# Performance work log

Measured on AMD Instinct MI355X. Metric: run time of the kernel, lower is better.

The kernel has to match this reference:

```python
import jax, jax.numpy as jnp
import numpy as np

B, S, H, FFN, E = 2, 2048, 1024, 4096, 8

def setup_inputs() -> dict:
    key = jax.random.key(0)
    k0, k1, k2, k3 = jax.random.split(key, 4)
    return {
        "hidden_states": jax.random.normal(k0, (B, S, H), dtype=jnp.float32),
        "Wr": jax.random.normal(k1, (H, E), dtype=jnp.float32) * 0.02,
        "br": jnp.zeros((E,), dtype=jnp.float32),
        "W1": jax.random.normal(k2, (E, H, FFN), dtype=jnp.float32) * 0.02,
        "W2": jax.random.normal(k3, (E, FFN, H), dtype=jnp.float32) * 0.02,
    }

def reference(hidden_states, Wr, br, W1, W2):
    b, s, h = hidden_states.shape
    x = hidden_states.reshape(-1, h)                      # [T, H]
    # sinkhorn routing branch in forward: sigmoid activation then top-1
    route = jax.nn.sigmoid(x @ Wr + br)                   # [T, E]
    max_prob = jnp.max(route, axis=1, keepdims=True)      # [T, 1]
    max_ind = jnp.argmax(route, axis=1)                   # [T] int
    out = jnp.zeros_like(x)
    n_experts = Wr.shape[1]
    for e in range(n_experts):  # small fixed expert set
        mask = (max_ind == e)[:, None].astype(x.dtype)    # [T, 1] dispatch mask
        # expert MLP: fc2(gelu(fc1(x))), no bias (add_bias_linear=False)
        y = jax.nn.gelu(x @ W1[e], approximate=False) @ W2[e]  # [T, H]
        out = out + mask * y                              # scatter-combine
    out = out * max_prob                                  # scale by router prob
    return out.reshape(b, s, h)
```

## Files before the change

### kernel.cpp

```cpp
#include <hip/hip_runtime.h>
#include <hip/hip_bf16.h>
#include <math.h>

#define TOK 4096
#define HD 1024
#define FD 4096
#define NE 8

typedef __attribute__((ext_vector_type(4))) float f32x4;
typedef __attribute__((ext_vector_type(8))) short s16x8;
typedef __attribute__((ext_vector_type(4))) unsigned short u16x4;

typedef const __attribute__((address_space(1))) void g_void;
typedef __attribute__((address_space(3))) void lds_void;

__device__ __forceinline__ unsigned short f2bf(float f) {
    union { float f; unsigned u; } v; v.f = f;
    unsigned r = v.u + 0x7FFFu + ((v.u >> 16) & 1u);
    return (unsigned short)(r >> 16);
}

__global__ void router_kernel(const float* __restrict__ x, const float* __restrict__ Wr,
                              const float* __restrict__ br, int* __restrict__ counts,
                              int* __restrict__ tlist, float* __restrict__ mprob,
                              unsigned short* __restrict__ xb) {
    const int lane = threadIdx.x & 63;
    const int t = blockIdx.x * 4 + (threadIdx.x >> 6);
    const float* xr = x + (size_t)t * HD;
    unsigned short* xbr = xb + (size_t)t * HD;
    float acc[NE];
#pragma unroll
    for (int e = 0; e < NE; ++e) acc[e] = 0.f;
    for (int h = lane; h < HD; h += 64) {
        float xv = xr[h];
        xbr[h] = f2bf(xv);
        f32x4 w0 = *(const f32x4*)(Wr + h * NE);
        f32x4 w1 = *(const f32x4*)(Wr + h * NE + 4);
        acc[0] += xv * w0.x; acc[1] += xv * w0.y; acc[2] += xv * w0.z; acc[3] += xv * w0.w;
        acc[4] += xv * w1.x; acc[5] += xv * w1.y; acc[6] += xv * w1.z; acc[7] += xv * w1.w;
    }
#pragma unroll
    for (int off = 32; off >= 1; off >>= 1)
#pragma unroll
        for (int e = 0; e < NE; ++e) acc[e] += __shfl_down(acc[e], off, 64);
    if (lane == 0) {
        float best = -1.f; int bi = 0;
#pragma unroll
        for (int e = 0; e < NE; ++e) {
            float r = 1.f / (1.f + expf(-(acc[e] + br[e])));
            if (r > best) { best = r; bi = e; }
        }
        mprob[t] = best;
        int pos = atomicAdd(&counts[bi], 1);
        tlist[bi * TOK + pos] = t;
    }
}

template<int K, int N>
__global__ __launch_bounds__(256)
void transpose_cast(const float* __restrict__ src, unsigned short* __restrict__ dst) {
    __shared__ unsigned short T[64][72];
    const int e = blockIdx.z;
    const int n0 = blockIdx.x * 64;
    const int k0 = blockIdx.y * 64;
    const int tid = threadIdx.x;
    {
        int c4 = (tid & 15) << 2;
#pragma unroll
        for (int it = 0; it < 4; ++it) {
            int r = (tid >> 4) + it * 16;
            f32x4 v = *(const f32x4*)(src + ((size_t)e * K + k0 + r) * N + n0 + c4);
            u16x4 p; p.x = f2bf(v.x); p.y = f2bf(v.y); p.z = f2bf(v.z); p.w = f2bf(v.w);
            *(u16x4*)&T[r][c4] = p;
        }
    }
    __syncthreads();
    {
        int c = tid >> 2;
        int q = tid & 3;
        s16x8 v0, v1;
#pragma unroll
        for (int j = 0; j < 8; ++j) { v0[j] = (short)T[q * 16 + j][c]; v1[j] = (short)T[q * 16 + 8 + j][c]; }
        unsigned short* op = dst + ((size_t)e * N + n0 + c) * K + k0 + q * 16;
        *(s16x8*)op = v0;
        *(s16x8*)(op + 8) = v1;
    }
}

template<int K, bool FC1, int KSPLIT>
__global__ __launch_bounds__(256, 4)
void expert_gemm(const unsigned short* __restrict__ Asrc, const unsigned short* __restrict__ Wt,
                 const int* __restrict__ counts, const int* __restrict__ tlist,
                 const float* __restrict__ mprob,
                 unsigned short* __restrict__ inter, float* __restrict__ out) {
    constexpr int NDIM = FC1 ? FD : HD;
    constexpr int KC = K / KSPLIT;
    const int e  = (KSPLIT == 1) ? blockIdx.z : (blockIdx.z & (NE - 1));
    const int ks = (KSPLIT == 1) ? 0 : ((int)blockIdx.z >> 3);
    const int kbase = ks * KC;
    const int cnt = counts[e];
    const int m0 = blockIdx.y * 128;
    if (m0 >= cnt) return;
    const int n0 = blockIdx.x * 128;

    __shared__ unsigned short Al[128 * 64];
    __shared__ unsigned short Bl[128 * 64];
    __shared__ int s_tok[128];
    __shared__ float s_prob[128];

    const int tid = threadIdx.x;
    if (tid < 128) {
        int m = m0 + tid;
        int tk = (m < cnt) ? tlist[e * TOK + m] : -1;
        s_tok[tid] = tk;
        s_prob[tid] = (!FC1 && tk >= 0) ? mprob[tk] : 0.f;
    }

    const int lane = tid & 63;
    const int wave = tid >> 6;
    const unsigned short* aptr[4];
    const unsigned short* bptr[4];
    {
        int lr = lane >> 3, g = lane & 7;
#pragma unroll
        for (int it = 0; it < 4; ++it) {
            int r = wave * 32 + it * 8 + lr;
            int kg = (g - r) & 7;
            int m = m0 + r;
            int tk = (m < cnt) ? tlist[e * TOK + m] : 0;
            aptr[it] = Asrc + (size_t)tk * K + kbase + kg * 8;
            bptr[it] = Wt + ((size_t)e * NDIM + n0 + r) * K + kbase + kg * 8;
        }
    }

    const int wrow = (wave >> 1) << 6;
    const int wcol = (wave & 1) << 6;
    const int lm = lane & 15, quad = lane >> 4;

    f32x4 acc[4][4] = {};

    for (int k0 = 0; k0 < KC; k0 += 64) {
        __syncthreads();
#pragma unroll
        for (int it = 0; it < 4; ++it) {
            __builtin_amdgcn_global_load_lds((g_void*)aptr[it],
                (lds_void*)&Al[wave * 2048 + it * 512], 16, 0, 0);
            __builtin_amdgcn_global_load_lds((g_void*)bptr[it],
                (lds_void*)&Bl[wave * 2048 + it * 512], 16, 0, 0);
            aptr[it] += 64; bptr[it] += 64;
        }
        __syncthreads();
#pragma unroll
        for (int kt = 0; kt < 2; ++kt) {
            s16x8 af[4], bf[4];
            int gk = (kt << 2) + quad;
#pragma unroll
            for (int mt = 0; mt < 4; ++mt) {
                int m = wrow + (mt << 4) + lm;
                af[mt] = *(const s16x8*)&Al[(m << 6) + (((gk + m) & 7) << 3)];
            }
#pragma unroll
            for (int nt = 0; nt < 4; ++nt) {
                int n = wcol + (nt << 4) + lm;
                bf[nt] = *(const s16x8*)&Bl[(n << 6) + (((gk + n) & 7) << 3)];
            }
#pragma unroll
            for (int mt = 0; mt < 4; ++mt)
#pragma unroll
                for (int nt = 0; nt < 4; ++nt)
                    acc[mt][nt] = __builtin_amdgcn_mfma_f32_16x16x32_bf16(
                        af[mt], bf[nt], acc[mt][nt], 0, 0, 0);
        }
    }

#pragma unroll
    for (int mt = 0; mt < 4; ++mt) {
#pragma unroll
        for (int r = 0; r < 4; ++r) {
            int row = wrow + (mt << 4) + (quad << 2) + r;
            if (m0 + row >= cnt) continue;
            int tk = s_tok[row];
            int colb = n0 + wcol + lm;
            if constexpr (FC1) {
#pragma unroll
                for (int nt = 0; nt < 4; ++nt) {
                    float v = acc[mt][nt][r];
                    float g = 0.5f * v * (1.f + erff(v * 0.70710678f));
                    inter[(size_t)tk * FD + colb + (nt << 4)] = f2bf(g);
                }
            } else {
                float p = s_prob[row];
#pragma unroll
                for (int nt = 0; nt < 4; ++nt)
                    atomicAdd(&out[(size_t)tk * HD + colb + (nt << 4)], acc[mt][nt][r] * p);
            }
        }
    }
}

extern "C" void kernel_launch(void* const* d_in, const int* in_sizes, int n_in,
                              void* d_out, int out_size, void* d_ws, size_t ws_size,
                              hipStream_t stream) {
    const float* x  = (const float*)d_in[0];
    const float* Wr = (const float*)d_in[1];
    const float* br = (const float*)d_in[2];
    const float* W1 = (const float*)d_in[3];
    const float* W2 = (const float*)d_in[4];
    float* out = (float*)d_out;

    char* ws = (char*)d_ws;
    int* counts           = (int*)ws;
    float* mprob          = (float*)(ws + 256);
    int* tlist            = (int*)(ws + 16640);
    unsigned short* xb    = (unsigned short*)(ws + 147712);
    unsigned short* inter = (unsigned short*)(ws + 8536320);
    unsigned short* Wt    = (unsigned short*)(ws + 42090752);

    hipMemsetAsync(counts, 0, NE * sizeof(int), stream);
    hipMemsetAsync(out, 0, (size_t)out_size * sizeof(float), stream);
    router_kernel<<<TOK / 4, 256, 0, stream>>>(x, Wr, br, counts, tlist, mprob, xb);

    transpose_cast<HD, FD><<<dim3(FD / 64, HD / 64, NE), 256, 0, stream>>>(W1, Wt);
    expert_gemm<HD, true, 1><<<dim3(FD / 128, TOK / 128, NE), 256, 0, stream>>>(
        xb, Wt, counts, tlist, mprob, inter, nullptr);

    transpose_cast<FD, HD><<<dim3(HD / 64, FD / 64, NE), 256, 0, stream>>>(W2, Wt);
    expert_gemm<FD, false, 4><<<dim3(HD / 128, TOK / 128, NE * 4), 256, 0, stream>>>(
        inter, Wt, counts, tlist, mprob, nullptr, out);
}
```

Baseline: 610.3 us.

## Fuse fp32 weight transpose-cast into expert GEMM with double-buffered A tiles

Drops the separate transpose_cast kernels. The expert GEMMs now load fp32 weight tiles directly into LDS and convert them to bf16 with v_cvt_pk_bf16_f32, writing a swizzled K-major layout. The A tile is double-buffered so the next global load overlaps the MFMA loop, and FC2 split-K goes from 4 to 2. This removes a full read and write pass over all expert weights (including weights for experts that get few tokens), but each M-tile block now reconverts its weight tiles and uses more LDS, which lowers occupancy to 2 blocks per CU.

```diff
diff --git a/kernel.cpp b/kernel.cpp
--- a/kernel.cpp
+++ b/kernel.cpp
@@ -9,7 +9,7 @@
 
 typedef __attribute__((ext_vector_type(4))) float f32x4;
 typedef __attribute__((ext_vector_type(8))) short s16x8;
-typedef __attribute__((ext_vector_type(4))) unsigned short u16x4;
+typedef __attribute__((ext_vector_type(4))) unsigned int u32x4;
 
 typedef const __attribute__((address_space(1))) void g_void;
 typedef __attribute__((address_space(3))) void lds_void;
@@ -18,6 +18,12 @@
     union { float f; unsigned u; } v; v.f = f;
     unsigned r = v.u + 0x7FFFu + ((v.u >> 16) & 1u);
     return (unsigned short)(r >> 16);
+}
+
+__device__ __forceinline__ unsigned cvt2(float a, float b) {
+    unsigned r;
+    asm("v_cvt_pk_bf16_f32 %0, %1, %2" : "=v"(r) : "v"(a), "v"(b));
+    return r;
 }
 
 __global__ void router_kernel(const float* __restrict__ x, const float* __restrict__ Wr,
@@ -56,46 +62,16 @@
     }
 }
 
-template<int K, int N>
-__global__ __launch_bounds__(256)
-void transpose_cast(const float* __restrict__ src, unsigned short* __restrict__ dst) {
-    __shared__ unsigned short T[64][72];
-    const int e = blockIdx.z;
-    const int n0 = blockIdx.x * 64;
-    const int k0 = blockIdx.y * 64;
-    const int tid = threadIdx.x;
-    {
-        int c4 = (tid & 15) << 2;
-#pragma unroll
-        for (int it = 0; it < 4; ++it) {
-            int r = (tid >> 4) + it * 16;
-            f32x4 v = *(const f32x4*)(src + ((size_t)e * K + k0 + r) * N + n0 + c4);
-            u16x4 p; p.x = f2bf(v.x); p.y = f2bf(v.y); p.z = f2bf(v.z); p.w = f2bf(v.w);
-            *(u16x4*)&T[r][c4] = p;
-        }
-    }
-    __syncthreads();
-    {
-        int c = tid >> 2;
-        int q = tid & 3;
-        s16x8 v0, v1;
-#pragma unroll
-        for (int j = 0; j < 8; ++j) { v0[j] = (short)T[q * 16 + j][c]; v1[j] = (short)T[q * 16 + 8 + j][c]; }
-        unsigned short* op = dst + ((size_t)e * N + n0 + c) * K + k0 + q * 16;
-        *(s16x8*)op = v0;
-        *(s16x8*)(op + 8) = v1;
-    }
-}
-
 template<int K, bool FC1, int KSPLIT>
-__global__ __launch_bounds__(256, 4)
-void expert_gemm(const unsigned short* __restrict__ Asrc, const unsigned short* __restrict__ Wt,
+__global__ __launch_bounds__(256, 2)
+void expert_gemm(const unsigned short* __restrict__ Asrc, const float* __restrict__ Wsrc,
                  const int* __restrict__ counts, const int* __restrict__ tlist,
                  const float* __restrict__ mprob,
                  unsigned short* __restrict__ inter, float* __restrict__ out) {
     constexpr int NDIM = FC1 ? FD : HD;
     constexpr int KC = K / KSPLIT;
-    const int e  = (KSPLIT == 1) ? blockIdx.z : (blockIdx.z & (NE - 1));
+    constexpr int NT = KC / 64;
+    const int e  = (KSPLIT == 1) ? blockIdx.z : ((int)blockIdx.z & (NE - 1));
     const int ks = (KSPLIT == 1) ? 0 : ((int)blockIdx.z >> 3);
     const int kbase = ks * KC;
     const int cnt = counts[e];
@@ -103,23 +79,15 @@
     if (m0 >= cnt) return;
     const int n0 = blockIdx.x * 128;
 
-    __shared__ unsigned short Al[128 * 64];
+    __shared__ unsigned short Al[2][128 * 64];
+    __shared__ float Braw[64 * 128];
     __shared__ unsigned short Bl[128 * 64];
-    __shared__ int s_tok[128];
-    __shared__ float s_prob[128];
 
     const int tid = threadIdx.x;
-    if (tid < 128) {
-        int m = m0 + tid;
-        int tk = (m < cnt) ? tlist[e * TOK + m] : -1;
-        s_tok[tid] = tk;
-        s_prob[tid] = (!FC1 && tk >= 0) ? mprob[tk] : 0.f;
-    }
-
     const int lane = tid & 63;
     const int wave = tid >> 6;
+
     const unsigned short* aptr[4];
-    const unsigned short* bptr[4];
     {
         int lr = lane >> 3, g = lane & 7;
 #pragma unroll
@@ -129,27 +97,65 @@
             int m = m0 + r;
             int tk = (m < cnt) ? tlist[e * TOK + m] : 0;
             aptr[it] = Asrc + (size_t)tk * K + kbase + kg * 8;
-            bptr[it] = Wt + ((size_t)e * NDIM + n0 + r) * K + kbase + kg * 8;
-        }
-    }
+        }
+    }
+    const float* bptr = Wsrc + ((size_t)e * K + kbase + wave * 16 + (lane >> 5)) * NDIM
+                        + n0 + ((lane & 31) << 2);
 
     const int wrow = (wave >> 1) << 6;
     const int wcol = (wave & 1) << 6;
     const int lm = lane & 15, quad = lane >> 4;
+    const int cg = tid >> 3;
+    const int gg = tid & 7;
 
     f32x4 acc[4][4] = {};
 
-    for (int k0 = 0; k0 < KC; k0 += 64) {
-        __syncthreads();
-#pragma unroll
-        for (int it = 0; it < 4; ++it) {
-            __builtin_amdgcn_global_load_lds((g_void*)aptr[it],
-                (lds_void*)&Al[wave * 2048 + it * 512], 16, 0, 0);
-            __builtin_amdgcn_global_load_lds((g_void*)bptr[it],
-                (lds_void*)&Bl[wave * 2048 + it * 512], 16, 0, 0);
-            aptr[it] += 64; bptr[it] += 64;
-        }
-        __syncthreads();
+#pragma unroll
+    for (int it = 0; it < 4; ++it)
+        __builtin_amdgcn_global_load_lds((g_void*)aptr[it],
+            (lds_void*)&Al[0][wave * 2048 + it * 512], 16, 0, 0);
+#pragma unroll
+    for (int L = 0; L < 8; ++L)
+        __builtin_amdgcn_global_load_lds((g_void*)(bptr + (size_t)(L * 2) * NDIM),
+            (lds_void*)&Braw[(wave * 16 + L * 2) * 128], 16, 0, 0);
+
+    for (int t = 0; t < NT; ++t) {
+        const int buf = t & 1;
+        asm volatile("s_waitcnt vmcnt(0) lgkmcnt(0)\n\ts_barrier" ::: "memory");
+
+        {
+            f32x4 v[8];
+#pragma unroll
+            for (int j = 0; j < 8; ++j)
+                v[j] = *(const f32x4*)&Braw[(gg * 8 + j) * 128 + (cg << 2)];
+#pragma unroll
+            for (int i = 0; i < 4; ++i) {
+                int n = (cg << 2) + i;
+                u32x4 q;
+                q.x = cvt2(v[0][i], v[1][i]);
+                q.y = cvt2(v[2][i], v[3][i]);
+                q.z = cvt2(v[4][i], v[5][i]);
+                q.w = cvt2(v[6][i], v[7][i]);
+                *(u32x4*)&Bl[(n << 6) + (((gg + n) & 7) << 3)] = q;
+            }
+        }
+        asm volatile("s_waitcnt lgkmcnt(0)\n\ts_barrier" ::: "memory");
+
+        if (t + 1 < NT) {
+#pragma unroll
+            for (int it = 0; it < 4; ++it) {
+                aptr[it] += 64;
+                __builtin_amdgcn_global_load_lds((g_void*)aptr[it],
+                    (lds_void*)&Al[buf ^ 1][wave * 2048 + it * 512], 16, 0, 0);
+            }
+            bptr += (size_t)64 * NDIM;
+#pragma unroll
+            for (int L = 0; L < 8; ++L)
+                __builtin_amdgcn_global_load_lds((g_void*)(bptr + (size_t)(L * 2) * NDIM),
+                    (lds_void*)&Braw[(wave * 16 + L * 2) * 128], 16, 0, 0);
+            __builtin_amdgcn_sched_barrier(0);
+        }
+
 #pragma unroll
         for (int kt = 0; kt < 2; ++kt) {
             s16x8 af[4], bf[4];
@@ -157,7 +163,7 @@
 #pragma unroll
             for (int mt = 0; mt < 4; ++mt) {
                 int m = wrow + (mt << 4) + lm;
-                af[mt] = *(const s16x8*)&Al[(m << 6) + (((gk + m) & 7) << 3)];
+                af[mt] = *(const s16x8*)&Al[buf][(m << 6) + (((gk + m) & 7) << 3)];
             }
 #pragma unroll
             for (int nt = 0; nt < 4; ++nt) {
@@ -179,7 +185,7 @@
         for (int r = 0; r < 4; ++r) {
             int row = wrow + (mt << 4) + (quad << 2) + r;
             if (m0 + row >= cnt) continue;
-            int tk = s_tok[row];
+            int tk = tlist[e * TOK + m0 + row];
             int colb = n0 + wcol + lm;
             if constexpr (FC1) {
 #pragma unroll
@@ -189,7 +195,7 @@
                     inter[(size_t)tk * FD + colb + (nt << 4)] = f2bf(g);
                 }
             } else {
-                float p = s_prob[row];
+                float p = mprob[tk];
 #pragma unroll
                 for (int nt = 0; nt < 4; ++nt)
                     atomicAdd(&out[(size_t)tk * HD + colb + (nt << 4)], acc[mt][nt][r] * p);
@@ -214,17 +220,14 @@
     int* tlist            = (int*)(ws + 16640);
     unsigned short* xb    = (unsigned short*)(ws + 147712);
     unsigned short* inter = (unsigned short*)(ws + 8536320);
-    unsigned short* Wt    = (unsigned short*)(ws + 42090752);
 
     hipMemsetAsync(counts, 0, NE * sizeof(int), stream);
     hipMemsetAsync(out, 0, (size_t)out_size * sizeof(float), stream);
     router_kernel<<<TOK / 4, 256, 0, stream>>>(x, Wr, br, counts, tlist, mprob, xb);
 
-    transpose_cast<HD, FD><<<dim3(FD / 64, HD / 64, NE), 256, 0, stream>>>(W1, Wt);
     expert_gemm<HD, true, 1><<<dim3(FD / 128, TOK / 128, NE), 256, 0, stream>>>(
-        xb, Wt, counts, tlist, mprob, inter, nullptr);
-
-    transpose_cast<FD, HD><<<dim3(HD / 64, FD / 64, NE), 256, 0, stream>>>(W2, Wt);
-    expert_gemm<FD, false, 4><<<dim3(HD / 128, TOK / 128, NE * 4), 256, 0, stream>>>(
-        inter, Wt, counts, tlist, mprob, nullptr, out);
-}
+        xb, W1, counts, tlist, mprob, inter, nullptr);
+
+    expert_gemm<FD, false, 2><<<dim3(HD / 128, TOK / 128, NE * 2), 256, 0, stream>>>(
+        inter, W2, counts, tlist, mprob, nullptr, out);
+}
```

After: 549.2 us. 1.11x faster.
